# Performance work log

Measured on AMD Instinct MI355X. Metric: run time of the kernel, lower is better.

Reference implementation:

```python
import jax, jax.numpy as jnp
import numpy as np

B, L = 2, 4096
D_MODEL = 1024
EXPAND = 2
D_INNER = EXPAND * D_MODEL            # 2048
HEADDIM = 64
NHEADS = D_INNER // HEADDIM           # 32
D_STATE = 128
NGROUPS = 1
D_CONV = 4
D_OUT = 1024
D_IN_PROJ = 2 * D_INNER + 2 * NGROUPS * D_STATE + NHEADS  # 4384
CONV_DIM = D_INNER + 2 * NGROUPS * D_STATE                # 2304
EPS = 1e-5


def setup_inputs() -> dict:
    key = jax.random.key(0)
    ks = jax.random.split(key, 8)
    x = jax.random.normal(ks[0], (B, L, D_MODEL), jnp.float32)
    in_proj_w = jax.random.normal(ks[1], (D_IN_PROJ, D_MODEL), jnp.float32) * (1.0 / np.sqrt(D_MODEL))
    conv_w = jax.random.normal(ks[2], (CONV_DIM, D_CONV), jnp.float32) * (1.0 / np.sqrt(D_CONV))
    conv_b = jnp.zeros((CONV_DIM,), jnp.float32)
    # dt_bias init as in the module: inverse-softplus of dt ~ LogUniform(1e-3, 1e-1)
    dt = jnp.exp(jax.random.uniform(ks[3], (NHEADS,)) * (np.log(0.1) - np.log(0.001)) + np.log(0.001))
    dt_bias = dt + jnp.log(-jnp.expm1(-dt))
    A_log = jnp.log(jax.random.uniform(ks[4], (NHEADS,), minval=1.0, maxval=16.0))
    Dp = jnp.ones((NHEADS,), jnp.float32)
    norm_w = jnp.ones((D_INNER,), jnp.float32)
    out_proj_w = jax.random.normal(ks[5], (D_OUT, D_INNER), jnp.float32) * (1.0 / np.sqrt(D_INNER))
    return {"x": x, "in_proj_w": in_proj_w, "conv_w": conv_w, "conv_b": conv_b,
            "dt_bias": dt_bias, "A_log": A_log, "Dp": Dp, "norm_w": norm_w,
            "out_proj_w": out_proj_w}


def _mamba_fwd(x, in_proj_w, conv_w, conv_b, dt_bias, A_log, Dp, norm_w, out_proj_w):
    # in_proj (no bias): (B,L,D_MODEL) -> (B,L,D_IN_PROJ)
    zxbcdt = jnp.einsum('bld,ed->ble', x, in_proj_w)
    z = zxbcdt[..., :D_INNER]                                  # gate branch
    xBC = zxbcdt[..., D_INNER:D_INNER + CONV_DIM]              # conv branch
    dt = zxbcdt[..., D_INNER + CONV_DIM:]                      # (B,L,H)
    # depthwise causal conv1d + SiLU
    xBC_t = jnp.transpose(xBC, (0, 2, 1))                      # (B, C, L)
    conv_out = jax.lax.conv_general_dilated(
        xBC_t, conv_w[:, None, :], window_strides=(1,),
        padding=[(D_CONV - 1, 0)],
        dimension_numbers=('NCH', 'OIH', 'NCH'),
        feature_group_count=CONV_DIM)
    xBC = jax.nn.silu(jnp.transpose(conv_out + conv_b[None, :, None], (0, 2, 1)))
    xs = xBC[..., :D_INNER].reshape(B, L, NHEADS, HEADDIM)     # (B,L,H,P)
    Bm = xBC[..., D_INNER:D_INNER + D_STATE]                   # (B,L,N), ngroups=1
    Cm = xBC[..., D_INNER + D_STATE:]                          # (B,L,N)
    A = -jnp.exp(A_log)                                        # (H,)
    dt = jax.nn.softplus(dt + dt_bias)                         # (B,L,H)
    dA = jnp.exp(dt * A)                                       # (B,L,H)

    def step(h, inp):
        dA_t, dt_t, B_t, x_t, C_t = inp
        # h: (B,H,P,N) selective state-space recurrence
        h = h * dA_t[:, :, None, None] + jnp.einsum('bh,bn,bhp->bhpn', dt_t, B_t, x_t)
        y = jnp.einsum('bhpn,bn->bhp', h, C_t)
        return h, y

    h0 = jnp.zeros((B, NHEADS, HEADDIM, D_STATE), xs.dtype)
    _, ys = jax.lax.scan(step, h0,
                         (jnp.swapaxes(dA, 0, 1), jnp.swapaxes(dt, 0, 1),
                          jnp.swapaxes(Bm, 0, 1), jnp.swapaxes(xs, 0, 1),
                          jnp.swapaxes(Cm, 0, 1)))
    y = jnp.swapaxes(ys, 0, 1) + Dp[None, None, :, None] * xs  # skip term D*x
    y = y.reshape(B, L, D_INNER)
    # gated RMSNorm (norm_before_gate=False): norm(y * silu(z)) * w
    y = y * jax.nn.silu(z)
    y = y * jax.lax.rsqrt(jnp.mean(y * y, axis=-1, keepdims=True) + EPS) * norm_w
    return jnp.einsum('bld,od->blo', y, out_proj_w)


def reference(x, in_proj_w, conv_w, conv_b, dt_bias, A_log, Dp, norm_w, out_proj_w):
    return _mamba_fwd(x, in_proj_w, conv_w, conv_b, dt_bias, A_log, Dp, norm_w, out_proj_w)
```

## Files before the change

kernel.cpp:

```cpp
#include <hip/hip_runtime.h>

#define LL 4096
#define DMODEL 1024
#define DINNER 2048
#define NHEADS 32
#define DSTATE 128
#define DINPROJ 4384
#define NZX 4352
#define CONVDIM 2304
#define ROWS 8192
#define Q 64
#define NCS 64
#define XCSEQ ((size_t)LL*CONVDIM)
#define LGSEQ ((size_t)NHEADS*NCS*Q)

typedef __attribute__((ext_vector_type(8))) __bf16 bf16x8;
typedef __attribute__((ext_vector_type(4))) float f32x4;

__device__ __forceinline__ float bf2f(ushort u){ union{uint i;float f;} v; v.i=(uint)u<<16; return v.f; }
__device__ __forceinline__ ushort f2bf(float f){ union{float f;uint i;} v; v.f=f; uint r=v.i+0x7fffu+((v.i>>16)&1u); return (ushort)(r>>16); }

__global__ __launch_bounds__(256) void cvt_all(
    const float4* __restrict__ x, uint4* __restrict__ xbf,
    const float4* __restrict__ ipw, ushort4* __restrict__ Wp,
    const float4* __restrict__ opw, uint4* __restrict__ opwb,
    const float* __restrict__ nw){
  int b = blockIdx.x, tid = threadIdx.x;
  if (b < 4096){
    long t = (long)b*256 + tid;
    float4 a = x[t*2], bb = x[t*2+1];
    ushort u[8] = { f2bf(a.x),f2bf(a.y),f2bf(a.z),f2bf(a.w),
                    f2bf(bb.x),f2bf(bb.y),f2bf(bb.z),f2bf(bb.w) };
    xbf[t] = *(uint4*)u;
  } else if (b < 4096 + 4480){
    int row = b - 4096;
    ushort4 o = make_ushort4(0,0,0,0);
    if (row < DINPROJ){
      float4 f = ipw[(size_t)row*256 + tid];
      o = make_ushort4(f2bf(f.x), f2bf(f.y), f2bf(f.z), f2bf(f.w));
    }
    Wp[(size_t)row*256 + tid] = o;
  } else {
    long t = (long)(b - 8576)*256 + tid;
    float4 a = opw[t*2], bb = opw[t*2+1];
    long e0 = t*8;
    float w0 = nw[(e0+0)&2047], w1 = nw[(e0+1)&2047], w2 = nw[(e0+2)&2047], w3 = nw[(e0+3)&2047];
    float w4 = nw[(e0+4)&2047], w5 = nw[(e0+5)&2047], w6 = nw[(e0+6)&2047], w7 = nw[(e0+7)&2047];
    ushort u[8] = { f2bf(a.x*w0),f2bf(a.y*w1),f2bf(a.z*w2),f2bf(a.w*w3),
                    f2bf(bb.x*w4),f2bf(bb.y*w5),f2bf(bb.z*w6),f2bf(bb.w*w7) };
    opwb[t] = *(uint4*)u;
  }
}

__device__ __forceinline__ void gld16(const void* g, void* l){
  __builtin_amdgcn_global_load_lds((const __attribute__((address_space(1))) void*)g,
                                   (__attribute__((address_space(3))) void*)l, 16, 0, 0);
}

#define GBM 128
#define GBN 128
#define GBK 32

__global__ __launch_bounds__(256) void gemm_tile(
    const ushort* __restrict__ A, int lda, long grow0, long rowmax,
    const ushort* __restrict__ W, int ldw,
    void* __restrict__ Cv, int ldc, int K, int obf, int swz, int q, int r,
    float* __restrict__ Cdt, const float* __restrict__ rowsc){
  __shared__ __align__(16) ushort As[2][GBM*GBK];
  __shared__ __align__(16) ushort Bs[2][GBN*GBK];
  __shared__ float scl[128];
  const int tid = threadIdx.x;
  const int lane = tid & 63, wave = tid >> 6;
  const int wm = wave >> 1, wn = wave & 1;
  int bx, by;
  if (swz){
    int wgid = blockIdx.y * gridDim.x + blockIdx.x;
    int xcd = wgid & 7, i = wgid >> 3;
    int vid = (xcd < r) ? xcd*(q+1) + i : r*(q+1) + (xcd - r)*q + i;
    int rows = gridDim.y;
    if (((rows & 7) == 0) && (r == 0)){
      int rp = rows >> 3;
      int lv = vid - xcd*q;
      by = xcd*rp + (lv % rp);
      bx = lv / rp;
    } else { by = vid / (int)gridDim.x; bx = vid % (int)gridDim.x; }
  } else { bx = blockIdx.x; by = blockIdx.y; }
  const int m0 = by * GBM, n0 = bx * GBN;

  const int srow = lane >> 2;
  const int scol = (((lane & 3) ^ ((lane >> 3) & 3)) * 8);
  long ra0 = grow0 + m0 + 16*wave + srow;      if (ra0 < 0) ra0 = 0; if (ra0 > rowmax) ra0 = rowmax;
  long ra1 = grow0 + m0 + 64 + 16*wave + srow; if (ra1 < 0) ra1 = 0; if (ra1 > rowmax) ra1 = rowmax;
  const ushort* gA0 = A + ra0*(long)lda + scol;
  const ushort* gA1 = A + ra1*(long)lda + scol;
  const ushort* gB0 = W + (size_t)(n0 + 16*wave + srow)*ldw + scol;
  const ushort* gB1 = W + (size_t)(n0 + 64 + 16*wave + srow)*ldw + scol;
  ushort* lA0 = &As[0][0] + (16*wave)*GBK;
  ushort* lA1 = &As[0][0] + (64 + 16*wave)*GBK;
  ushort* lB0 = &Bs[0][0] + (16*wave)*GBK;
  ushort* lB1 = &Bs[0][0] + (64 + 16*wave)*GBK;

  const int fr = lane & 15, quad = lane >> 4;
  const int es = ((quad ^ ((fr >> 1) & 3)) * 8);
  f32x4 acc[4][4] = {};

#define STAGE(buf, ko) { \
    gld16(gA0 + (ko), lA0 + (buf)*(GBM*GBK)); \
    gld16(gA1 + (ko), lA1 + (buf)*(GBM*GBK)); \
    gld16(gB0 + (ko), lB0 + (buf)*(GBN*GBK)); \
    gld16(gB1 + (ko), lB1 + (buf)*(GBN*GBK)); }

  STAGE(0, 0);
  if (rowsc && tid < 128){
    long rr = grow0 + m0 + tid; if (rr < 0) rr = 0; if (rr > rowmax) rr = rowmax;
    const float* pr = rowsc + (size_t)rr*128;
    float s = 0.f;
    #pragma unroll
    for (int h=0;h<32;h++) s += pr[h];
    scl[tid] = rsqrtf(s*(1.f/(float)DINNER) + 1e-5f);
  }
  __syncthreads();
  int cur = 0;
  const int nst = K / GBK;
  for (int s = 0; s < nst; ++s){
    if (s + 1 < nst) STAGE(cur^1, (s+1)*GBK);
    const ushort* Ab = &As[cur][0];
    const ushort* Bb = &Bs[cur][0];
    bf16x8 af[4], bw[4];
    #pragma unroll
    for (int i=0;i<4;i++) af[i] = *(const bf16x8*)(Ab + (wm*64 + i*16 + fr)*GBK + es);
    #pragma unroll
    for (int j=0;j<4;j++) bw[j] = *(const bf16x8*)(Bb + (wn*64 + j*16 + fr)*GBK + es);
    #pragma unroll
    for (int i=0;i<4;i++)
      #pragma unroll
      for (int j=0;j<4;j++)
        acc[i][j] = __builtin_amdgcn_mfma_f32_16x16x32_bf16(af[i], bw[j], acc[i][j], 0,0,0);
    if (s + 1 < nst){ __syncthreads(); cur ^= 1; }
  }
#undef STAGE
  if (rowsc){
    #pragma unroll
    for (int i=0;i<4;i++){
      #pragma unroll
      for (int rr=0;rr<4;rr++){
        float sv = scl[wm*64 + i*16 + quad*4 + rr];
        #pragma unroll
        for (int j=0;j<4;j++) acc[i][j][rr] *= sv;
      }
    }
  }
  if (Cdt && n0 >= NZX){
    int nb = n0 - NZX;
    #pragma unroll
    for (int i=0;i<4;i++)
      #pragma unroll
      for (int j=0;j<4;j++){
        size_t base = (size_t)(m0 + wm*64 + i*16 + quad*4)*128 + (nb + wn*64 + j*16 + fr);
        #pragma unroll
        for (int rr=0;rr<4;rr++)
          Cdt[base + (size_t)rr*128] = acc[i][j][rr];
      }
  } else if (obf){
    ushort* Cb = (ushort*)Cv;
    #pragma unroll
    for (int i=0;i<4;i++)
      #pragma unroll
      for (int j=0;j<4;j++){
        size_t base = (size_t)(m0 + wm*64 + i*16 + quad*4)*ldc + (n0 + wn*64 + j*16 + fr);
        #pragma unroll
        for (int rr=0;rr<4;rr++)
          Cb[base + (size_t)rr*ldc] = f2bf(acc[i][j][rr]);
      }
  } else {
    float* Cf = (float*)Cv;
    #pragma unroll
    for (int i=0;i<4;i++)
      #pragma unroll
      for (int j=0;j<4;j++){
        size_t base = (size_t)(m0 + wm*64 + i*16 + quad*4)*ldc + (n0 + wn*64 + j*16 + fr);
        #pragma unroll
        for (int rr=0;rr<4;rr++)
          Cf[base + (size_t)rr*ldc] = acc[i][j][rr];
      }
  }
}

__global__ __launch_bounds__(256) void conv8(const ushort* __restrict__ zxh,
    const float* __restrict__ cw, const float* __restrict__ cb,
    ushort* __restrict__ xconv, int l0, long base){
  int z = blockIdx.y;
  long bb = base + (long)z*LL;
  ushort* xc = xconv + (size_t)z*XCSEQ;
  int id = blockIdx.x*256 + threadIdx.x;
  int g = id % 288, band = id / 288;
  int c = g*8;
  float w[8][4], bias[8];
  #pragma unroll
  for (int i=0;i<8;i++){
    bias[i] = cb[c+i];
    #pragma unroll
    for (int j=0;j<4;j++) w[i][j] = cw[(c+i)*4+j];
  }
  float in[7][8];
  #pragma unroll
  for (int k=0;k<7;k++){
    int lrow = l0 + band*4 - 3 + k;
    if (lrow < 0){
      #pragma unroll
      for (int i=0;i<8;i++) in[k][i] = 0.f;
    } else {
      uint4 v = *(const uint4*)(zxh + (size_t)(bb + band*4 - 3 + k)*NZX + DINNER + c);
      const ushort* us = (const ushort*)&v;
      #pragma unroll
      for (int i=0;i<8;i++) in[k][i] = bf2f(us[i]);
    }
  }
  #pragma unroll
  for (int r=0;r<4;r++){
    ushort o[8];
    #pragma unroll
    for (int i=0;i<8;i++){
      float a = bias[i];
      #pragma unroll
      for (int j=0;j<4;j++) a = fmaf(in[r+j][i], w[i][j], a);
      float v = a / (1.f + expf(-a));
      o[i] = f2bf(v);
    }
    *(uint4*)(xc + (size_t)(band*4 + r)*CONVDIM + c) = *(uint4*)o;
  }
}

__global__ __launch_bounds__(256) void scan_pre2(const ushort* __restrict__ xcv0,
    const float* __restrict__ dtraw, long dtrow0,
    const float* __restrict__ dtb, const float* __restrict__ alog,
    ushort* __restrict__ gbuf0, ushort* __restrict__ gbuf1,
    float* __restrict__ lgbuf0, int cslot0){
  const int c = blockIdx.x, h = blockIdx.y, z = blockIdx.z;
  const ushort* xcv = xcv0 + (size_t)z*XCSEQ;
  const long dtr0 = dtrow0 + (long)z*LL;
  ushort* gbuf = z ? gbuf1 : gbuf0;
  float* lgbuf = lgbuf0 + (size_t)z*LGSEQ;
  const int cslot = cslot0 + c;
  const int tid = threadIdx.x, lane = tid & 63, w = tid >> 6;
  const int l15 = lane & 15, quad = lane >> 4, kq = quad*8;
  __shared__ float wsx[Q];
  __shared__ __align__(16) ushort XT[64*72];
  __shared__ __align__(16) ushort BTw[128*72];
  const int c0 = c*Q;
  if (tid < 64){
    float xv = dtraw[(size_t)(dtr0 + c0 + tid)*128 + h] + dtb[h];
    float sp = (xv > 20.f) ? xv : log1pf(expf(xv));
    float la = sp * (-expf(alog[h]));
    float v = la;
    #pragma unroll
    for (int off=1; off<64; off<<=1){ float u = __shfl_up(v, off); if (tid >= off) v += u; }
    float tot = __shfl(v, 63);
    wsx[tid] = __expf(tot - v)*sp;
    lgbuf[((size_t)h*NCS + cslot)*Q + tid] = v;
  }
  __syncthreads();
  { int s = tid>>2, pb = (tid&3)*16;
    const ushort* src = xcv + (size_t)(c0+s)*CONVDIM + h*64 + pb;
    ushort tmp[16];
    *(uint4*)tmp     = *(const uint4*)src;
    *(uint4*)(tmp+8) = *(const uint4*)(src+8);
    #pragma unroll
    for (int i=0;i<16;i++) XT[(pb+i)*72 + s] = tmp[i];
  }
  { int s = tid>>2, nb4 = (tid&3)*32;
    const ushort* src = xcv + (size_t)(c0+s)*CONVDIM + DINNER + nb4;
    float wv = wsx[s];
    ushort tmp[32];
    #pragma unroll
    for (int v4=0;v4<4;v4++) *(uint4*)(tmp+v4*8) = *(const uint4*)(src+v4*8);
    #pragma unroll
    for (int i=0;i<32;i++) BTw[(nb4+i)*72 + s] = f2bf(bf2f(tmp[i])*wv);
  }
  __syncthreads();
  f32x4 g[8] = {};
  #pragma unroll
  for (int kb=0;kb<2;kb++){
    bf16x8 afr = *(const bf16x8*)(XT + (16*w + l15)*72 + kb*32 + kq);
    #pragma unroll
    for (int j=0;j<8;j++){
      bf16x8 bfr = *(const bf16x8*)(BTw + (16*j + l15)*72 + kb*32 + kq);
      g[j] = __builtin_amdgcn_mfma_f32_16x16x32_bf16(afr, bfr, g[j], 0,0,0);
    }
  }
  __syncthreads();
  ushort* gst = &BTw[0];
  #pragma unroll
  for (int j=0;j<8;j++)
    #pragma unroll
    for (int r=0;r<4;r++)
      gst[(16*w + quad*4 + r)*136 + 16*j + l15] = f2bf(g[j][r]);
  __syncthreads();
  { int row = tid >> 2, seg = tid & 3;
    const ushort* gs = gst + row*136 + seg*32;
    uint4 a = *(const uint4*)(gs);
    uint4 b = *(const uint4*)(gs + 8);
    uint4 c2 = *(const uint4*)(gs + 16);
    uint4 d = *(const uint4*)(gs + 24);
    ushort* gdst = gbuf + ((size_t)h*NCS + cslot)*8192 + row*128 + seg*32;
    *(uint4*)gdst = a;
    *(uint4*)(gdst + 8) = b;
    *(uint4*)(gdst + 16) = c2;
    *(uint4*)(gdst + 24) = d;
  }
}

__global__ __launch_bounds__(256) void scan_carry2(ushort* __restrict__ g0p,
    ushort* __restrict__ g1p, const float* __restrict__ lgbuf0, int ncs){
  const int qtr = blockIdx.x, h = blockIdx.y, z = blockIdx.z;
  ushort* gh = z ? g1p : g0p;
  const float* lgbuf = lgbuf0 + (size_t)z*LGSEQ;
  const int tid = threadIdx.x;
  __shared__ float es[NCS];
  if (tid < ncs) es[tid] = __expf(lgbuf[((size_t)h*NCS + tid)*Q + 63]);
  __syncthreads();
  float hreg[8] = {0.f,0.f,0.f,0.f,0.f,0.f,0.f,0.f};
  ushort* p0 = gh + (size_t)h*NCS*8192 + qtr*2048 + tid*8;
  uint4 g0 = *(const uint4*)p0;
  uint4 g1 = *(const uint4*)(p0 + 8192);
  for (int c = 0; c < ncs; ++c){
    ushort* pc = p0 + (size_t)c*8192;
    uint4 gc = g0; g0 = g1;
    if (c + 2 < ncs) g1 = *(const uint4*)(pc + 2*8192);
    ushort u[8];
    #pragma unroll
    for (int i=0;i<8;i++) u[i] = f2bf(hreg[i]);
    *(uint4*)pc = *(uint4*)u;
    float e = es[c];
    const ushort* gs = (const ushort*)&gc;
    #pragma unroll
    for (int i=0;i<8;i++) hreg[i] = fmaf(hreg[i], e, bf2f(gs[i]));
  }
}

__global__ __launch_bounds__(256) void scan_y2(ushort* __restrict__ xcv0,
    const ushort* __restrict__ zxh,
    float* __restrict__ dtraw, long dtrow0,
    const float* __restrict__ dtb, const float* __restrict__ alog,
    const float* __restrict__ lgbuf0, const ushort* __restrict__ gbuf0,
    const ushort* __restrict__ gbuf1, const float* __restrict__ Dp, int cslot0){
  const int c = blockIdx.x, h = blockIdx.y, z = blockIdx.z;
  ushort* xcv = xcv0 + (size_t)z*XCSEQ;
  const long dtr0 = dtrow0 + (long)z*LL;
  const ushort* gbuf = z ? gbuf1 : gbuf0;
  const float* lgbuf = lgbuf0 + (size_t)z*LGSEQ;
  const int cslot = cslot0 + c;
  const int tid = threadIdx.x, lane = tid & 63, w = tid >> 6;
  const int l15 = lane & 15, quad = lane >> 4, kq = quad*8;
  __shared__ float lg[Q], dts[Q], els[Q];
  __shared__ __align__(16) ushort XT[64*72];
  __shared__ __align__(16) ushort Cc[64*136];
  __shared__ __align__(16) ushort Bp[64*136];
  const int c0 = c*Q;
  if (tid < 64){
    float v = lgbuf[((size_t)h*NCS + cslot)*Q + tid];
    lg[tid] = v;
    els[tid] = __expf(v);
    float xv = dtraw[(size_t)(dtr0 + c0 + tid)*128 + h] + dtb[h];
    dts[tid] = (xv > 20.f) ? xv : log1pf(expf(xv));
  }
  { int s = tid>>2, pb = (tid&3)*16;
    const ushort* src = xcv + (size_t)(c0+s)*CONVDIM + h*64 + pb;
    ushort tmp[16];
    *(uint4*)tmp     = *(const uint4*)src;
    *(uint4*)(tmp+8) = *(const uint4*)(src+8);
    #pragma unroll
    for (int i=0;i<16;i++) XT[(pb+i)*72 + s] = tmp[i];
  }
  { int row = tid >> 2, seg = tid & 3;
    const ushort* bsrc = xcv + (size_t)(c0 + row)*CONVDIM + DINNER + seg*32;
    const ushort* csrc = bsrc + DSTATE;
    #pragma unroll
    for (int k=0;k<4;k++){
      *(uint4*)(Bp + row*136 + seg*32 + k*8) = *(const uint4*)(bsrc + k*8);
      *(uint4*)(Cc + row*136 + seg*32 + k*8) = *(const uint4*)(csrc + k*8);
    }
  }
  __syncthreads();
  f32x4 sac[4] = {};
  #pragma unroll
  for (int kb=0;kb<4;kb++){
    bf16x8 afr = *(const bf16x8*)(Cc + (16*w + l15)*136 + kb*32 + kq);
    #pragma unroll
    for (int j=0;j<4;j++){
      bf16x8 bfr = *(const bf16x8*)(Bp + (16*j + l15)*136 + kb*32 + kq);
      sac[j] = __builtin_amdgcn_mfma_f32_16x16x32_bf16(afr, bfr, sac[j], 0,0,0);
    }
  }
  __syncthreads();
  #pragma unroll
  for (int j=0;j<4;j++){
    int s = 16*j + l15;
    float lgs = lg[s], dtss = dts[s];
    #pragma unroll
    for (int r=0;r<4;r++){
      int t = 16*w + quad*4 + r;
      float val = (t >= s) ? sac[j][r]*__expf(lg[t]-lgs)*dtss : 0.f;
      Bp[t*72 + s] = f2bf(val);
    }
  }
  __syncthreads();
  float yv[4][4];
  {
    const float dph = Dp[h];
    bf16x8 hb[4], xb[2];
    const ushort* hrow = gbuf + ((size_t)h*NCS + cslot)*8192 + (16*w + l15)*128;
    #pragma unroll
    for (int kb=0;kb<4;kb++) hb[kb] = *(const bf16x8*)(hrow + kb*32 + kq);
    #pragma unroll
    for (int kb=0;kb<2;kb++) xb[kb] = *(const bf16x8*)(XT + (16*w + l15)*72 + kb*32 + kq);
    #pragma unroll
    for (int i=0;i<4;i++){
      f32x4 y2 = {};
      #pragma unroll
      for (int kb=0;kb<4;kb++){
        bf16x8 afr = *(const bf16x8*)(Cc + (16*i + l15)*136 + kb*32 + kq);
        y2 = __builtin_amdgcn_mfma_f32_16x16x32_bf16(afr, hb[kb], y2, 0,0,0);
      }
      f32x4 y1 = {};
      #pragma unroll
      for (int kb=0;kb<2;kb++){
        bf16x8 afr = *(const bf16x8*)(Bp + (16*i + l15)*72 + kb*32 + kq);
        y1 = __builtin_amdgcn_mfma_f32_16x16x32_bf16(afr, xb[kb], y1, 0,0,0);
      }
      int p = 16*w + l15;
      #pragma unroll
      for (int r=0;r<4;r++){
        int t = 16*i + quad*4 + r;
        float xv = bf2f(XT[p*72 + t]);
        yv[i][r] = y1[r] + els[t]*y2[r] + dph*xv;
      }
    }
  }
  {
    const ushort* zcol = zxh + (size_t)(dtr0 + c0)*NZX + h*64 + (16*w + l15);
    #pragma unroll
    for (int i=0;i<4;i++)
      #pragma unroll
      for (int r=0;r<4;r++){
        int t = 16*i + quad*4 + r;
        float zz = bf2f(zcol[(size_t)t*NZX]);
        yv[i][r] *= zz / (1.f + expf(-zz));
      }
  }
  __syncthreads();
  {
    int p = 16*w + l15;
    #pragma unroll
    for (int i=0;i<4;i++)
      #pragma unroll
      for (int r=0;r<4;r++)
        Bp[(16*i + quad*4 + r)*72 + p] = f2bf(yv[i][r]);
  }
  __syncthreads();
  { int t = tid >> 2, seg = tid & 3;
    uint4 a = *(const uint4*)(Bp + t*72 + seg*16);
    uint4 b = *(const uint4*)(Bp + t*72 + seg*16 + 8);
    ushort* od = xcv + (size_t)(c0 + t)*CONVDIM + h*64 + seg*16;
    *(uint4*)od = a;
    *(uint4*)(od + 8) = b;
    const ushort* ya = (const ushort*)&a;
    const ushort* yb2 = (const ushort*)&b;
    float ss = 0.f;
    #pragma unroll
    for (int i=0;i<8;i++){ float v1 = bf2f(ya[i]); float v2 = bf2f(yb2[i]); ss = fmaf(v1,v1, fmaf(v2,v2, ss)); }
    ss += __shfl_xor(ss, 1);
    ss += __shfl_xor(ss, 2);
    if (seg == 0)
      dtraw[(size_t)(dtr0 + c0 + t)*128 + 64 + h] = ss;
  }
}

extern "C" void kernel_launch(void* const* d_in, const int* in_sizes, int n_in,
                              void* d_out, int out_size, void* d_ws, size_t ws_size,
                              hipStream_t stream) {
  const float* x    = (const float*)d_in[0];
  const float* ipw  = (const float*)d_in[1];
  const float* cw   = (const float*)d_in[2];
  const float* cb   = (const float*)d_in[3];
  const float* dtb  = (const float*)d_in[4];
  const float* alog = (const float*)d_in[5];
  const float* Dp   = (const float*)d_in[6];
  const float* nw   = (const float*)d_in[7];
  const float* opw  = (const float*)d_in[8];
  char* ws = (char*)d_ws;
  size_t off = 0;
  ushort* Wp    = (ushort*)(ws + off); off += (size_t)4480*DMODEL*2;
  ushort* opwb  = (ushort*)(ws + off); off += (size_t)DMODEL*DINNER*2;
  float*  dtraw = (float*)(ws + off);  off += (size_t)ROWS*128*4;
  ushort* zxbh  = (ushort*)(ws + off); off += (size_t)ROWS*NZX*2;

  const size_t lg_b  = LGSEQ*4;
  const size_t xc_b  = XCSEQ*2;
  const size_t xc_fb = (size_t)1024*CONVDIM*2;
  const size_t gb_b  = (size_t)NHEADS*NCS*8192*2;

  size_t needA = off + 2*lg_b + 2*xc_b + gb_b;
  size_t needB = off + lg_b + xc_b + gb_b;
  int mode = (ws_size >= needA) ? 2 : (ws_size >= needB ? 1 : 0);

  float* lgbuf = (float*)(ws + off); off += (mode == 2) ? 2*lg_b : lg_b;
  ushort* xconv = (ushort*)(ws + off);
  off += (mode == 2) ? 2*xc_b : (mode == 1 ? xc_b : xc_fb);
  ushort* xbf  = (ushort*)(ws + off);
  ushort* gbuf0 = (ushort*)(ws + off);
  ushort* gbuf1 = (mode == 2) ? (ushort*)d_out : gbuf0;

  cvt_all<<<9600, 256, 0, stream>>>((const float4*)x, (uint4*)xbf,
                                    (const float4*)ipw, (ushort4*)Wp,
                                    (const float4*)opw, (uint4*)opwb, nw);

  gemm_tile<<<dim3(35, 64), 256, 0, stream>>>(
      xbf, DMODEL, 0, (long)ROWS-1, Wp, DMODEL,
      zxbh, NZX, DMODEL, 1, 1, 280, 0, dtraw, nullptr);

  if (mode == 2){
    conv8<<<dim3(288*(LL/4)/256, 2), 256, 0, stream>>>(zxbh, cw, cb, xconv, 0, 0);
    scan_pre2<<<dim3(NCS, NHEADS, 2), 256, 0, stream>>>(
        xconv, dtraw, 0, dtb, alog, gbuf0, gbuf1, lgbuf, 0);
    scan_carry2<<<dim3(4, NHEADS, 2), 256, 0, stream>>>(gbuf0, gbuf1, lgbuf, NCS);
    scan_y2<<<dim3(NCS, NHEADS, 2), 256, 0, stream>>>(
        xconv, zxbh, dtraw, 0, dtb, alog, lgbuf, gbuf0, gbuf1, Dp, 0);
    gemm_tile<<<dim3(8, 64), 256, 0, stream>>>(
        xconv, CONVDIM, 0, (long)ROWS-1, opwb, DINNER,
        (float*)d_out, DMODEL, DINNER, 0, 1, 64, 0, nullptr, dtraw + 64);
  } else if (mode == 1){
    for (int b = 0; b < 2; ++b){
      long row0 = (long)b*LL;
      conv8<<<dim3(288*(LL/4)/256, 1), 256, 0, stream>>>(zxbh, cw, cb, xconv, 0, row0);
      scan_pre2<<<dim3(NCS, NHEADS, 1), 256, 0, stream>>>(
          xconv, dtraw, row0, dtb, alog, gbuf0, gbuf0, lgbuf, 0);
      scan_carry2<<<dim3(4, NHEADS, 1), 256, 0, stream>>>(gbuf0, gbuf0, lgbuf, NCS);
      scan_y2<<<dim3(NCS, NHEADS, 1), 256, 0, stream>>>(
          xconv, zxbh, dtraw, row0, dtb, alog, lgbuf, gbuf0, gbuf0, Dp, 0);
      gemm_tile<<<dim3(8, 32), 256, 0, stream>>>(
          xconv, CONVDIM, 0, (long)LL-1, opwb, DINNER,
          (float*)d_out + (size_t)row0*DMODEL, DMODEL, DINNER, 0, 1, 32, 0,
          nullptr, dtraw + 64 + (size_t)row0*128);
    }
  } else {
    for (int b = 0; b < 2; ++b){
      long row0 = (long)b*LL;
      for (int ckl = 0; ckl < 4; ++ckl){
        long g0 = row0 + (long)ckl*1024;
        conv8<<<dim3(288*(1024/4)/256, 1), 256, 0, stream>>>(zxbh, cw, cb, xconv, ckl*1024, g0);
        scan_pre2<<<dim3(16, NHEADS, 1), 256, 0, stream>>>(
            xconv, dtraw, g0, dtb, alog, gbuf0, gbuf0, lgbuf, ckl*16);
      }
      scan_carry2<<<dim3(4, NHEADS, 1), 256, 0, stream>>>(gbuf0, gbuf0, lgbuf, NCS);
      for (int ckl = 0; ckl < 4; ++ckl){
        long g0 = row0 + (long)ckl*1024;
        conv8<<<dim3(288*(1024/4)/256, 1), 256, 0, stream>>>(zxbh, cw, cb, xconv, ckl*1024, g0);
        scan_y2<<<dim3(16, NHEADS, 1), 256, 0, stream>>>(
            xconv, zxbh, dtraw, g0, dtb, alog, lgbuf, gbuf0, gbuf0, Dp, ckl*16);
        gemm_tile<<<dim3(8, 8), 256, 0, stream>>>(
            xconv, CONVDIM, 0, 1023L, opwb, DINNER,
            (float*)d_out + (size_t)g0*DMODEL, DMODEL, DINNER, 0, 1, 8, 0,
            nullptr, dtraw + 64 + (size_t)g0*128);
      }
    }
  }
}
```

Before: 384.0 us.

## Fuse x-channel causal conv+SiLU into scan kernels, keep separate conv for B/C only

```diff
diff --git a/kernel.cpp b/kernel.cpp
--- a/kernel.cpp
+++ b/kernel.cpp
@@ -186,15 +186,15 @@
   }
 }
 
-__global__ __launch_bounds__(256) void conv8(const ushort* __restrict__ zxh,
+__global__ __launch_bounds__(256) void convBC(const ushort* __restrict__ zxh,
     const float* __restrict__ cw, const float* __restrict__ cb,
     ushort* __restrict__ xconv, int l0, long base){
   int z = blockIdx.y;
   long bb = base + (long)z*LL;
   ushort* xc = xconv + (size_t)z*XCSEQ;
   int id = blockIdx.x*256 + threadIdx.x;
-  int g = id % 288, band = id / 288;
-  int c = g*8;
+  int g = id & 31, band = id >> 5;
+  int c = 2048 + g*8;
   float w[8][4], bias[8];
   #pragma unroll
   for (int i=0;i<8;i++){
@@ -231,8 +231,38 @@
   }
 }
 
-__global__ __launch_bounds__(256) void scan_pre2(const ushort* __restrict__ xcv0,
-    const float* __restrict__ dtraw, long dtrow0,
+__device__ __forceinline__ void conv_x16(const ushort* __restrict__ zxh,
+    const float* __restrict__ cw, const float* __restrict__ cb,
+    long grow, int lrow0, int ch0, ushort* __restrict__ XT, int s, int pb){
+  const ushort* base = zxh + grow*NZX + DINNER + ch0;
+  float acc[16];
+  #pragma unroll
+  for (int i=0;i<16;i++) acc[i] = cb[ch0+i];
+  #pragma unroll
+  for (int k=0;k<4;k++){
+    if (lrow0 + k >= 0){
+      uint4 v0 = *(const uint4*)(base + (size_t)k*NZX);
+      uint4 v1 = *(const uint4*)(base + (size_t)k*NZX + 8);
+      const ushort* u0 = (const ushort*)&v0;
+      const ushort* u1 = (const ushort*)&v1;
+      #pragma unroll
+      for (int i=0;i<8;i++){
+        acc[i]   = fmaf(bf2f(u0[i]), cw[(ch0+i)*4 + k], acc[i]);
+        acc[8+i] = fmaf(bf2f(u1[i]), cw[(ch0+8+i)*4 + k], acc[8+i]);
+      }
+    }
+  }
+  #pragma unroll
+  for (int i=0;i<16;i++){
+    float v = acc[i];
+    XT[(pb+i)*72 + s] = f2bf(v / (1.f + expf(-v)));
+  }
+}
+
+__global__ __launch_bounds__(256) void scan_pre2(const ushort* __restrict__ zxh,
+    const ushort* __restrict__ xcv0,
+    const float* __restrict__ dtraw, long dtrow0, int l0,
+    const float* __restrict__ cw, const float* __restrict__ cb,
     const float* __restrict__ dtb, const float* __restrict__ alog,
     ushort* __restrict__ gbuf0, ushort* __restrict__ gbuf1,
     float* __restrict__ lgbuf0, int cslot0){
@@ -259,15 +289,10 @@
     wsx[tid] = __expf(tot - v)*sp;
     lgbuf[((size_t)h*NCS + cslot)*Q + tid] = v;
   }
-  __syncthreads();
   { int s = tid>>2, pb = (tid&3)*16;
-    const ushort* src = xcv + (size_t)(c0+s)*CONVDIM + h*64 + pb;
-    ushort tmp[16];
-    *(uint4*)tmp     = *(const uint4*)src;
-    *(uint4*)(tmp+8) = *(const uint4*)(src+8);
-    #pragma unroll
-    for (int i=0;i<16;i++) XT[(pb+i)*72 + s] = tmp[i];
-  }
+    conv_x16(zxh, cw, cb, dtr0 + c0 + s - 3, l0 + c0 + s - 3, h*64 + pb, XT, s, pb);
+  }
+  __syncthreads();
   { int s = tid>>2, nb4 = (tid&3)*32;
     const ushort* src = xcv + (size_t)(c0+s)*CONVDIM + DINNER + nb4;
     float wv = wsx[s];
@@ -340,7 +365,8 @@
 
 __global__ __launch_bounds__(256) void scan_y2(ushort* __restrict__ xcv0,
     const ushort* __restrict__ zxh,
-    float* __restrict__ dtraw, long dtrow0,
+    float* __restrict__ dtraw, long dtrow0, int l0,
+    const float* __restrict__ cw, const float* __restrict__ cb,
     const float* __restrict__ dtb, const float* __restrict__ alog,
     const float* __restrict__ lgbuf0, const ushort* __restrict__ gbuf0,
     const ushort* __restrict__ gbuf1, const float* __restrict__ Dp, int cslot0){
@@ -365,12 +391,7 @@
     dts[tid] = (xv > 20.f) ? xv : log1pf(expf(xv));
   }
   { int s = tid>>2, pb = (tid&3)*16;
-    const ushort* src = xcv + (size_t)(c0+s)*CONVDIM + h*64 + pb;
-    ushort tmp[16];
-    *(uint4*)tmp     = *(const uint4*)src;
-    *(uint4*)(tmp+8) = *(const uint4*)(src+8);
-    #pragma unroll
-    for (int i=0;i<16;i++) XT[(pb+i)*72 + s] = tmp[i];
+    conv_x16(zxh, cw, cb, dtr0 + c0 + s - 3, l0 + c0 + s - 3, h*64 + pb, XT, s, pb);
   }
   { int row = tid >> 2, seg = tid & 3;
     const ushort* bsrc = xcv + (size_t)(c0 + row)*CONVDIM + DINNER + seg*32;
@@ -520,24 +541,24 @@
       zxbh, NZX, DMODEL, 1, 1, 280, 0, dtraw, nullptr);
 
   if (mode == 2){
-    conv8<<<dim3(288*(LL/4)/256, 2), 256, 0, stream>>>(zxbh, cw, cb, xconv, 0, 0);
+    convBC<<<dim3(32*(LL/4)/256, 2), 256, 0, stream>>>(zxbh, cw, cb, xconv, 0, 0);
     scan_pre2<<<dim3(NCS, NHEADS, 2), 256, 0, stream>>>(
-        xconv, dtraw, 0, dtb, alog, gbuf0, gbuf1, lgbuf, 0);
+        zxbh, xconv, dtraw, 0, 0, cw, cb, dtb, alog, gbuf0, gbuf1, lgbuf, 0);
     scan_carry2<<<dim3(4, NHEADS, 2), 256, 0, stream>>>(gbuf0, gbuf1, lgbuf, NCS);
     scan_y2<<<dim3(NCS, NHEADS, 2), 256, 0, stream>>>(
-        xconv, zxbh, dtraw, 0, dtb, alog, lgbuf, gbuf0, gbuf1, Dp, 0);
+        xconv, zxbh, dtraw, 0, 0, cw, cb, dtb, alog, lgbuf, gbuf0, gbuf1, Dp, 0);
     gemm_tile<<<dim3(8, 64), 256, 0, stream>>>(
         xconv, CONVDIM, 0, (long)ROWS-1, opwb, DINNER,
         (float*)d_out, DMODEL, DINNER, 0, 1, 64, 0, nullptr, dtraw + 64);
   } else if (mode == 1){
     for (int b = 0; b < 2; ++b){
       long row0 = (long)b*LL;
-      conv8<<<dim3(288*(LL/4)/256, 1), 256, 0, stream>>>(zxbh, cw, cb, xconv, 0, row0);
+      convBC<<<dim3(32*(LL/4)/256, 1), 256, 0, stream>>>(zxbh, cw, cb, xconv, 0, row0);
       scan_pre2<<<dim3(NCS, NHEADS, 1), 256, 0, stream>>>(
-          xconv, dtraw, row0, dtb, alog, gbuf0, gbuf0, lgbuf, 0);
+          zxbh, xconv, dtraw, row0, 0, cw, cb, dtb, alog, gbuf0, gbuf0, lgbuf, 0);
       scan_carry2<<<dim3(4, NHEADS, 1), 256, 0, stream>>>(gbuf0, gbuf0, lgbuf, NCS);
       scan_y2<<<dim3(NCS, NHEADS, 1), 256, 0, stream>>>(
-          xconv, zxbh, dtraw, row0, dtb, alog, lgbuf, gbuf0, gbuf0, Dp, 0);
+          xconv, zxbh, dtraw, row0, 0, cw, cb, dtb, alog, lgbuf, gbuf0, gbuf0, Dp, 0);
       gemm_tile<<<dim3(8, 32), 256, 0, stream>>>(
           xconv, CONVDIM, 0, (long)LL-1, opwb, DINNER,
           (float*)d_out + (size_t)row0*DMODEL, DMODEL, DINNER, 0, 1, 32, 0,
@@ -548,16 +569,16 @@
       long row0 = (long)b*LL;
       for (int ckl = 0; ckl < 4; ++ckl){
         long g0 = row0 + (long)ckl*1024;
-        conv8<<<dim3(288*(1024/4)/256, 1), 256, 0, stream>>>(zxbh, cw, cb, xconv, ckl*1024, g0);
+        convBC<<<dim3(32*(1024/4)/256, 1), 256, 0, stream>>>(zxbh, cw, cb, xconv, ckl*1024, g0);
         scan_pre2<<<dim3(16, NHEADS, 1), 256, 0, stream>>>(
-            xconv, dtraw, g0, dtb, alog, gbuf0, gbuf0, lgbuf, ckl*16);
+            zxbh, xconv, dtraw, g0, ckl*1024, cw, cb, dtb, alog, gbuf0, gbuf0, lgbuf, ckl*16);
       }
       scan_carry2<<<dim3(4, NHEADS, 1), 256, 0, stream>>>(gbuf0, gbuf0, lgbuf, NCS);
       for (int ckl = 0; ckl < 4; ++ckl){
         long g0 = row0 + (long)ckl*1024;
-        conv8<<<dim3(288*(1024/4)/256, 1), 256, 0, stream>>>(zxbh, cw, cb, xconv, ckl*1024, g0);
+        convBC<<<dim3(32*(1024/4)/256, 1), 256, 0, stream>>>(zxbh, cw, cb, xconv, ckl*1024, g0);
         scan_y2<<<dim3(16, NHEADS, 1), 256, 0, stream>>>(
-            xconv, zxbh, dtraw, g0, dtb, alog, lgbuf, gbuf0, gbuf0, Dp, ckl*16);
+            xconv, zxbh, dtraw, g0, ckl*1024, cw, cb, dtb, alog, lgbuf, gbuf0, gbuf0, Dp, ckl*16);
         gemm_tile<<<dim3(8, 8), 256, 0, stream>>>(
             xconv, CONVDIM, 0, 1023L, opwb, DINNER,
             (float*)d_out + (size_t)g0*DMODEL, DMODEL, DINNER, 0, 1, 8, 0,
```

Result: slower. 407.1 us (+6.0%).
